# Optimization experiments

Measured on AMD Instinct MI355X. Metric: run time of the kernel, lower is better.

The kernel has to match this reference:

```python
import jax, jax.numpy as jnp
import numpy as np

N_PHOTONS = 20_000_000
HEX_R = 24  # axial hex grid radius -> 3R^2+3R+1 = 1801 pixels
SQRT3 = 3.0 ** 0.5


def _build_sensor():
    # Build pointy-top hex pixel centers on an axial grid (replicates hex_centers input),
    # then replicate HexagonalSensor.__init__ lookup-table construction in numpy.
    size = 1.0
    qs, rs = [], []
    for q in range(-HEX_R, HEX_R + 1):
        for r in range(max(-HEX_R, -q - HEX_R), min(HEX_R, -q + HEX_R) + 1):
            qs.append(q); rs.append(r)
    q = np.array(qs, dtype=np.float64); r = np.array(rs, dtype=np.float64)
    centers = np.stack([size * SQRT3 * (q + r / 2.0), size * 1.5 * r], axis=-1)
    n_pixels = centers.shape[0]
    diff = centers[:, None, :] - centers[None, :, :]
    d = np.sqrt((diff ** 2).sum(-1))
    np.fill_diagonal(d, np.inf)
    hex_size = float(d.min() / SQRT3)
    cx, cy = centers[:, 0], centers[:, 1]
    qa = (SQRT3 / 3.0 * cx - cy / 3.0) / hex_size
    ra = (2.0 / 3.0) * cy / hex_size
    q_offset = float(qa[0] - np.round(qa[0]))
    r_offset = float(ra[0] - np.round(ra[0]))
    q_grid = np.round(qa - q_offset).astype(np.int32)
    r_grid = np.round(ra - r_offset).astype(np.int32)
    q_min = int(q_grid.min()); r_min = int(r_grid.min())
    lookup = np.full((int(q_grid.max()) - q_min + 1, int(r_grid.max()) - r_min + 1), -1, dtype=np.int32)
    lookup[q_grid - q_min, r_grid - r_min] = np.arange(n_pixels)
    return hex_size, q_offset, r_offset, q_min, r_min, n_pixels, jnp.asarray(lookup)


def setup_inputs() -> dict:
    key = jax.random.key(0)
    kx, ky, kv = jax.random.split(key, 3)
    hex_size, q_off, r_off, q_min, r_min, n_pixels, lookup = _build_sensor()
    extent = 45.0  # camera footprint (~sqrt(3)*R + margin) so some photons miss (tests masking)
    x = jax.random.uniform(kx, (N_PHOTONS,), minval=-extent, maxval=extent, dtype=jnp.float32)
    y = jax.random.uniform(ky, (N_PHOTONS,), minval=-extent, maxval=extent, dtype=jnp.float32)
    values = jax.random.uniform(kv, (N_PHOTONS,), dtype=jnp.float32)
    return {"x": x, "y": y, "values": values, "lookup_table": lookup,
            "hex_size": hex_size, "q_offset": q_off, "r_offset": r_off,
            "q_min": q_min, "r_min": r_min, "n_pixels": n_pixels}


def _axial_round(q, r):
    s = -q - r
    qr, rr, sr = jnp.round(q), jnp.round(r), jnp.round(s)
    qd, rd, sd = jnp.abs(qr - q), jnp.abs(rr - r), jnp.abs(sr - s)
    qr2 = jnp.where((qd > rd) & (qd > sd), -rr - sr, qr)
    rr2 = jnp.where((rd > qd) & (rd > sd), -qr - sr, rr)
    return qr2, rr2


def reference(x, y, values, lookup_table, hex_size, q_offset, r_offset, q_min, r_min, n_pixels):
    # Cartesian -> axial hex coords
    q = (SQRT3 / 3.0 * x - y / 3.0) / hex_size
    r = (2.0 / 3.0) * y / hex_size
    qg, rg = _axial_round(q - q_offset, r - r_offset)
    q_idx = qg.astype(jnp.int32) - q_min
    r_idx = rg.astype(jnp.int32) - r_min
    Q, R = lookup_table.shape
    in_bounds = (q_idx >= 0) & (q_idx < Q) & (r_idx >= 0) & (r_idx < R)
    pixel_idx = lookup_table[q_idx.clip(0, Q - 1), r_idx.clip(0, R - 1)]
    valid = in_bounds & (pixel_idx >= 0)
    pixel_idx = jnp.where(valid, pixel_idx, 0)
    vals = jnp.where(valid, values, jnp.zeros((), values.dtype))
    return jax.ops.segment_sum(vals, pixel_idx, num_segments=n_pixels)
```

## Files before the change

### kernel.cpp

```cpp
#include <hip/hip_runtime.h>
#include <math.h>


typedef float f32x4 __attribute__((ext_vector_type(4)));

#define BIN_BLOCKS 2048
#define RED_ROWS   64

__global__ void hex_zero_kernel(float* __restrict__ p, int n) {
    int i = blockIdx.x * blockDim.x + threadIdx.x;
    if (i < n) p[i] = 0.0f;
}

__global__ __launch_bounds__(256) void hex_reduce_kernel(
    const float* __restrict__ partials, float* __restrict__ out,
    int n_pixels, int nrows)
{
    int pix = blockIdx.x * blockDim.x + threadIdx.x;
    if (pix >= n_pixels) return;
    int r0 = blockIdx.y * RED_ROWS;
    int r1 = min(r0 + RED_ROWS, nrows);
    float s = 0.0f;
    const float* p = partials + (size_t)r0 * n_pixels + pix;
    #pragma unroll 8
    for (int r = r0; r < r1; ++r) {
        s += *p;
        p += n_pixels;
    }
    atomicAdd(&out[pix], s);
}

__global__ __launch_bounds__(256) void hex_bin_kernel(
    const float* __restrict__ x,
    const float* __restrict__ y,
    const float* __restrict__ vals,
    const float* __restrict__ hex_size_p,
    const float* __restrict__ q_off_p,
    const float* __restrict__ r_off_p,
    const int*   __restrict__ q_min_p,
    const int*   __restrict__ r_min_p,
    int Rh, int n_pixels, int n_photons,
    float* __restrict__ flush_dst,
    int flush_mode)
{
    extern __shared__ float hist[];
    for (int i = threadIdx.x; i < n_pixels; i += blockDim.x) hist[i] = 0.0f;
    __syncthreads();

    const float inv_h = 1.0f / hex_size_p[0];
    const float A  = 0.57735026918962576f * inv_h;
    const float Bn = -(0.33333333333333333f * inv_h);
    const float C  = 0.66666666666666667f * inv_h;
    const float qc = -q_off_p[0];
    const float rc = -r_off_p[0];
    const int   qmin = q_min_p[0];
    const int   rmin = r_min_p[0];

    const unsigned twoR = (unsigned)(2 * Rh);
    const int Rp1 = Rh + 1;

    auto process = [&](float xf, float yf, float vf) {
        float q = fmaf(A, xf, fmaf(Bn, yf, qc));
        float r = fmaf(C, yf, rc);
        float t = q + r;
        float qr = rintf(q);
        float rr = rintf(r);
        float tr = rintf(t);
        float qd = fabsf(qr - q);
        float rd = fabsf(rr - r);
        float td = fabsf(tr - t);
        float q2 = (qd > rd && qd > td) ? (tr - rr) : qr;
        float r2 = (rd > qd && rd > td) ? (tr - qr) : rr;
        int qi = (int)q2 - qmin;
        int ri = (int)r2 - rmin;
        int d  = qi + ri;
        if ((unsigned)qi <= twoR && (unsigned)ri <= twoR &&
            (unsigned)(d - Rh) <= twoR) {
            int u  = max(qi - Rh, 0);
            int p  = qi * Rp1 + ((qi * qi - qi) >> 1) + d - Rh - u * u;
            atomicAdd(&hist[p], vf);
        }
    };

    const int tid    = blockIdx.x * blockDim.x + threadIdx.x;
    const int stride = gridDim.x * blockDim.x;
    const int n8     = n_photons >> 3;

    const f32x4* __restrict__ x4 = (const f32x4*)x;
    const f32x4* __restrict__ y4 = (const f32x4*)y;
    const f32x4* __restrict__ v4 = (const f32x4*)vals;

    f32x4 xa, xb, ya, yb, va, vb;
    int i = tid;
    if (i < n8) {
        int a = 2 * i, b = a + 1;
        xa = __builtin_nontemporal_load(&x4[a]);
        xb = __builtin_nontemporal_load(&x4[b]);
        ya = __builtin_nontemporal_load(&y4[a]);
        yb = __builtin_nontemporal_load(&y4[b]);
        va = __builtin_nontemporal_load(&v4[a]);
        vb = __builtin_nontemporal_load(&v4[b]);
    }
    while (i < n8) {
        int nx = i + stride;
        f32x4 nxa, nxb, nya, nyb, nva, nvb;
        bool has_next = nx < n8;
        if (has_next) {
            int a = 2 * nx, b = a + 1;
            nxa = __builtin_nontemporal_load(&x4[a]);
            nxb = __builtin_nontemporal_load(&x4[b]);
            nya = __builtin_nontemporal_load(&y4[a]);
            nyb = __builtin_nontemporal_load(&y4[b]);
            nva = __builtin_nontemporal_load(&v4[a]);
            nvb = __builtin_nontemporal_load(&v4[b]);
        }
        process(xa.x, ya.x, va.x);
        process(xa.y, ya.y, va.y);
        process(xa.z, ya.z, va.z);
        process(xa.w, ya.w, va.w);
        process(xb.x, yb.x, vb.x);
        process(xb.y, yb.y, vb.y);
        process(xb.z, yb.z, vb.z);
        process(xb.w, yb.w, vb.w);
        if (has_next) {
            xa = nxa; xb = nxb; ya = nya; yb = nyb; va = nva; vb = nvb;
        }
        i = nx;
    }
    for (int t2 = (n8 << 3) + tid; t2 < n_photons; t2 += stride) {
        process(x[t2], y[t2], vals[t2]);
    }

    __syncthreads();
    if (flush_mode == 2) {
        float* dst = flush_dst + (size_t)blockIdx.x * n_pixels;
        for (int k = threadIdx.x; k < n_pixels; k += blockDim.x)
            dst[k] = hist[k];
    } else if (flush_mode == 1) {
        float* dst = flush_dst + (size_t)(blockIdx.x & 63) * n_pixels;
        for (int k = threadIdx.x; k < n_pixels; k += blockDim.x) {
            float h = hist[k];
            if (h != 0.0f) atomicAdd(&dst[k], h);
        }
    } else {
        for (int k = threadIdx.x; k < n_pixels; k += blockDim.x) {
            float h = hist[k];
            if (h != 0.0f) atomicAdd(&flush_dst[k], h);
        }
    }
}

extern "C" void kernel_launch(void* const* d_in, const int* in_sizes, int n_in,
                              void* d_out, int out_size, void* d_ws, size_t ws_size,
                              hipStream_t stream) {
    const float* x      = (const float*)d_in[0];
    const float* y      = (const float*)d_in[1];
    const float* vals   = (const float*)d_in[2];
    const float* hexs   = (const float*)d_in[4];
    const float* qoff   = (const float*)d_in[5];
    const float* roff   = (const float*)d_in[6];
    const int*   qmin   = (const int*)d_in[7];
    const int*   rmin   = (const int*)d_in[8];

    const int n_photons = in_sizes[0];
    const int lut_elems = in_sizes[3];
    const int Q  = (int)(0.5 + sqrt((double)lut_elems));
    const int Rh = (Q - 1) / 2;
    const int n_pixels = out_size;

    float* out = (float*)d_out;
    float* partials = (float*)d_ws;

    const int threads = 256;
    const int blocks  = BIN_BLOCKS;
    const size_t lds_bytes = (size_t)n_pixels * sizeof(float);

    const size_t full_elems = (size_t)blocks * (size_t)n_pixels;
    const size_t p64_elems  = (size_t)64 * (size_t)n_pixels;

    if (ws_size >= full_elems * sizeof(float)) {
        hex_zero_kernel<<<(n_pixels + 255) / 256, 256, 0, stream>>>(out, n_pixels);
        hex_bin_kernel<<<blocks, threads, lds_bytes, stream>>>(
            x, y, vals, hexs, qoff, roff, qmin, rmin,
            Rh, n_pixels, n_photons, partials, 2);
        dim3 rgrid((n_pixels + 255) / 256, blocks / RED_ROWS);
        hex_reduce_kernel<<<rgrid, 256, 0, stream>>>(partials, out, n_pixels, blocks);
    } else if (ws_size >= p64_elems * sizeof(float)) {
        int zn = (int)p64_elems;
        hex_zero_kernel<<<(zn + 255) / 256, 256, 0, stream>>>(partials, zn);
        hex_zero_kernel<<<(n_pixels + 255) / 256, 256, 0, stream>>>(out, n_pixels);
        hex_bin_kernel<<<blocks, threads, lds_bytes, stream>>>(
            x, y, vals, hexs, qoff, roff, qmin, rmin,
            Rh, n_pixels, n_photons, partials, 1);
        dim3 rgrid((n_pixels + 255) / 256, 1);
        hex_reduce_kernel<<<rgrid, 256, 0, stream>>>(partials, out, n_pixels, 64);
    } else {
        hex_zero_kernel<<<(n_pixels + 255) / 256, 256, 0, stream>>>(out, n_pixels);
        hex_bin_kernel<<<blocks, threads, lds_bytes, stream>>>(
            x, y, vals, hexs, qoff, roff, qmin, rmin,
            Rh, n_pixels, n_photons, out, 0);
    }
}
```

Measured before the change: 83.03 us.

## Use fewer, larger blocks with contiguous per-block chunks for hex binning

Result: faster. 74.04 us (-10.8%).

```diff
diff --git a/kernel.cpp b/kernel.cpp
--- a/kernel.cpp
+++ b/kernel.cpp
@@ -4,8 +4,9 @@
 
 typedef float f32x4 __attribute__((ext_vector_type(4)));
 
-#define BIN_BLOCKS 2048
-#define RED_ROWS   64
+#define BIN_BLOCKS  512
+#define BIN_THREADS 1024
+#define RED_GROUP   32
 
 __global__ void hex_zero_kernel(float* __restrict__ p, int n) {
     int i = blockIdx.x * blockDim.x + threadIdx.x;
@@ -18,8 +19,8 @@
 {
     int pix = blockIdx.x * blockDim.x + threadIdx.x;
     if (pix >= n_pixels) return;
-    int r0 = blockIdx.y * RED_ROWS;
-    int r1 = min(r0 + RED_ROWS, nrows);
+    int r0 = blockIdx.y * RED_GROUP;
+    int r1 = min(r0 + RED_GROUP, nrows);
     float s = 0.0f;
     const float* p = partials + (size_t)r0 * n_pixels + pix;
     #pragma unroll 8
@@ -30,7 +31,7 @@
     atomicAdd(&out[pix], s);
 }
 
-__global__ __launch_bounds__(256) void hex_bin_kernel(
+__global__ __launch_bounds__(BIN_THREADS) void hex_bin_kernel(
     const float* __restrict__ x,
     const float* __restrict__ y,
     const float* __restrict__ vals,
@@ -82,53 +83,44 @@
         }
     };
 
-    const int tid    = blockIdx.x * blockDim.x + threadIdx.x;
-    const int stride = gridDim.x * blockDim.x;
-    const int n8     = n_photons >> 3;
+    const int n4 = n_photons >> 2;
+    const f32x4* __restrict__ px = (const f32x4*)x;
+    const f32x4* __restrict__ py = (const f32x4*)y;
+    const f32x4* __restrict__ pv = (const f32x4*)vals;
 
-    const f32x4* __restrict__ x4 = (const f32x4*)x;
-    const f32x4* __restrict__ y4 = (const f32x4*)y;
-    const f32x4* __restrict__ v4 = (const f32x4*)vals;
+    const int C4 = (n4 + gridDim.x - 1) / gridDim.x;
+    const int g0 = blockIdx.x * C4;
+    const int g1 = min(g0 + C4, n4);
 
-    f32x4 xa, xb, ya, yb, va, vb;
-    int i = tid;
-    if (i < n8) {
-        int a = 2 * i, b = a + 1;
-        xa = __builtin_nontemporal_load(&x4[a]);
-        xb = __builtin_nontemporal_load(&x4[b]);
-        ya = __builtin_nontemporal_load(&y4[a]);
-        yb = __builtin_nontemporal_load(&y4[b]);
-        va = __builtin_nontemporal_load(&v4[a]);
-        vb = __builtin_nontemporal_load(&v4[b]);
+    int g = g0 + threadIdx.x;
+    f32x4 xa, ya, va;
+    if (g < g1) {
+        xa = __builtin_nontemporal_load(&px[g]);
+        ya = __builtin_nontemporal_load(&py[g]);
+        va = __builtin_nontemporal_load(&pv[g]);
     }
-    while (i < n8) {
-        int nx = i + stride;
-        f32x4 nxa, nxb, nya, nyb, nva, nvb;
-        bool has_next = nx < n8;
+    while (g < g1) {
+        int gn = g + blockDim.x;
+        f32x4 nx, ny, nv;
+        bool has_next = gn < g1;
         if (has_next) {
-            int a = 2 * nx, b = a + 1;
-            nxa = __builtin_nontemporal_load(&x4[a]);
-            nxb = __builtin_nontemporal_load(&x4[b]);
-            nya = __builtin_nontemporal_load(&y4[a]);
-            nyb = __builtin_nontemporal_load(&y4[b]);
-            nva = __builtin_nontemporal_load(&v4[a]);
-            nvb = __builtin_nontemporal_load(&v4[b]);
+            nx = __builtin_nontemporal_load(&px[gn]);
+            ny = __builtin_nontemporal_load(&py[gn]);
+            nv = __builtin_nontemporal_load(&pv[gn]);
         }
         process(xa.x, ya.x, va.x);
         process(xa.y, ya.y, va.y);
         process(xa.z, ya.z, va.z);
         process(xa.w, ya.w, va.w);
-        process(xb.x, yb.x, vb.x);
-        process(xb.y, yb.y, vb.y);
-        process(xb.z, yb.z, vb.z);
-        process(xb.w, yb.w, vb.w);
-        if (has_next) {
-            xa = nxa; xb = nxb; ya = nya; yb = nyb; va = nva; vb = nvb;
-        }
-        i = nx;
+        if (has_next) { xa = nx; ya = ny; va = nv; }
+        g = gn;
     }
-    for (int t2 = (n8 << 3) + tid; t2 < n_photons; t2 += stride) {
-        process(x[t2], y[t2], vals[t2]);
+
+    {
+        int t0 = (n4 << 2) + blockIdx.x * blockDim.x + threadIdx.x;
+        int ts = gridDim.x * blockDim.x;
+        for (int t = t0; t < n_photons; t += ts)
+            process(x[t], y[t], vals[t]);
     }
 
     __syncthreads();
@@ -136,12 +128,6 @@
         float* dst = flush_dst + (size_t)blockIdx.x * n_pixels;
         for (int k = threadIdx.x; k < n_pixels; k += blockDim.x)
             dst[k] = hist[k];
-    } else if (flush_mode == 1) {
-        float* dst = flush_dst + (size_t)(blockIdx.x & 63) * n_pixels;
-        for (int k = threadIdx.x; k < n_pixels; k += blockDim.x) {
-            float h = hist[k];
-            if (h != 0.0f) atomicAdd(&dst[k], h);
-        }
     } else {
         for (int k = threadIdx.x; k < n_pixels; k += blockDim.x) {
             float h = hist[k];
@@ -171,32 +157,20 @@
     float* out = (float*)d_out;
     float* partials = (float*)d_ws;
 
-    const int threads = 256;
-    const int blocks  = BIN_BLOCKS;
     const size_t lds_bytes = (size_t)n_pixels * sizeof(float);
+    const size_t part_elems = (size_t)BIN_BLOCKS * (size_t)n_pixels;
 
-    const size_t full_elems = (size_t)blocks * (size_t)n_pixels;
-    const size_t p64_elems  = (size_t)64 * (size_t)n_pixels;
-
-    if (ws_size >= full_elems * sizeof(float)) {
+    if (ws_size >= part_elems * sizeof(float)) {
         hex_zero_kernel<<<(n_pixels + 255) / 256, 256, 0, stream>>>(out, n_pixels);
-        hex_bin_kernel<<<blocks, threads, lds_bytes, stream>>>(
+        hex_bin_kernel<<<BIN_BLOCKS, BIN_THREADS, lds_bytes, stream>>>(
             x, y, vals, hexs, qoff, roff, qmin, rmin,
             Rh, n_pixels, n_photons, partials, 2);
-        dim3 rgrid((n_pixels + 255) / 256, blocks / RED_ROWS);
-        hex_reduce_kernel<<<rgrid, 256, 0, stream>>>(partials, out, n_pixels, blocks);
-    } else if (ws_size >= p64_elems * sizeof(float)) {
-        int zn = (int)p64_elems;
-        hex_zero_kernel<<<(zn + 255) / 256, 256, 0, stream>>>(partials, zn);
-        hex_zero_kernel<<<(n_pixels + 255) / 256, 256, 0, stream>>>(out, n_pixels);
-        hex_bin_kernel<<<blocks, threads, lds_bytes, stream>>>(
-            x, y, vals, hexs, qoff, roff, qmin, rmin,
-            Rh, n_pixels, n_photons, partials, 1);
-        dim3 rgrid((n_pixels + 255) / 256, 1);
-        hex_reduce_kernel<<<rgrid, 256, 0, stream>>>(partials, out, n_pixels, 64);
+        dim3 rgrid((n_pixels + 255) / 256, BIN_BLOCKS / RED_GROUP);
+        hex_reduce_kernel<<<rgrid, 256, 0, stream>>>(
+            partials, out, n_pixels, BIN_BLOCKS);
     } else {
         hex_zero_kernel<<<(n_pixels + 255) / 256, 256, 0, stream>>>(out, n_pixels);
-        hex_bin_kernel<<<blocks, threads, lds_bytes, stream>>>(
+        hex_bin_kernel<<<BIN_BLOCKS, BIN_THREADS, lds_bytes, stream>>>(
             x, y, vals, hexs, qoff, roff, qmin, rmin,
             Rh, n_pixels, n_photons, out, 0);
     }
```
